# Kernel tuning notes

Measured on AMD Instinct MI355X. Metric: run time of the kernel, lower is better.

## Reference

```python
import jax, jax.numpy as jnp
import numpy as np

H = 16  # n_heads

def setup_inputs() -> dict:
    key = jax.random.key(0)
    ks = jax.random.split(key, 11)
    B, L, D = 2, 2048, 1024
    w = 1.0 / np.sqrt(D).astype(np.float32)
    return {
        "query": jax.random.normal(ks[0], (B, L, D), jnp.float32),
        "key":   jax.random.normal(ks[1], (B, L, D), jnp.float32),
        "value": jax.random.normal(ks[2], (B, L, D), jnp.float32),
        "Wq": jax.random.normal(ks[3], (D, D), jnp.float32) * w,
        "bq": jax.random.normal(ks[4], (D,), jnp.float32) * 0.01,
        "Wk": jax.random.normal(ks[5], (D, D), jnp.float32) * w,
        "bk": jax.random.normal(ks[6], (D,), jnp.float32) * 0.01,
        "Wv": jax.random.normal(ks[7], (D, D), jnp.float32) * w,
        "bv": jax.random.normal(ks[8], (D,), jnp.float32) * 0.01,
        "Wo": jax.random.normal(ks[9], (D, D), jnp.float32) * w,
        "bo": jax.random.normal(ks[10], (D,), jnp.float32) * 0.01,
        "masksize": 256,
    }

def reference(query, key, value, Wq, bq, Wk, bk, Wv, bv, Wo, bo, masksize):
    B, L, D = query.shape
    d_k = D // H
    scale = 1.0 / np.sqrt(d_k).astype(np.float32)

    def proj(x, W, b):
        # nn.Linear: x @ W.T + b, then [B,L,H,d_k] -> [B,H,L,d_k]
        return (x @ W.T + b).reshape(B, L, H, d_k).transpose(0, 2, 1, 3)

    q = proj(query, Wq, bq)
    k = proj(key, Wk, bk)
    v = proj(value, Wv, bv)

    # Sliding-window float mask (faithful to original: a 0/1 FLOAT tensor is
    # passed as attn_mask to SDPA, so it is ADDED to scores, not -inf-masked).
    half = masksize // 2
    i = jnp.arange(L)[:, None]
    j = jnp.arange(L)[None, :]
    band = (jnp.abs(i - j) <= half).astype(q.dtype)  # [L, L]

    scores = jnp.einsum('bhqd,bhkd->bhqk', q, k) * scale + band  # [B,H,L,L]
    attn = jax.nn.softmax(scores, axis=-1)
    out = jnp.einsum('bhqk,bhkd->bhqd', attn, v)  # [B,H,L,d_k]
    out = out.transpose(0, 2, 1, 3).reshape(B, L, D)
    return out @ Wo.T + bo
```

## Files before the change

kernel.cpp:

```cpp
#include <hip/hip_runtime.h>
#include <hip/hip_bf16.h>

#define Hh 16
#define Ll 2048
#define Dd 1024
#define DK 64
#define Mm 4096
#define Kk 1024
#define Nn 1024

typedef short bf16x8 __attribute__((ext_vector_type(8)));
typedef float f32x4 __attribute__((ext_vector_type(4)));

static __device__ __forceinline__ unsigned short f2bf(float f) {
    union { __hip_bfloat16 b; unsigned short u; } cv;
    cv.b = __float2bfloat16(f);
    return cv.u;
}

static __device__ __forceinline__ unsigned packtr(float a, float b) {
    return __builtin_amdgcn_perm(__builtin_bit_cast(unsigned, b),
                                 __builtin_bit_cast(unsigned, a), 0x07060302u);
}

static __device__ __forceinline__ float fexp2(float x) {
    return __builtin_amdgcn_exp2f(x);
}

static __device__ __forceinline__ void glds16(const ushort* g, ushort* l) {
    __builtin_amdgcn_global_load_lds((const __attribute__((address_space(1))) unsigned int*)g,
                                     (__attribute__((address_space(3))) unsigned int*)l,
                                     16, 0, 0);
}

__global__ __launch_bounds__(256) void cast_all(
    const float* __restrict__ q, const float* __restrict__ k, const float* __restrict__ v,
    const float* __restrict__ wq, const float* __restrict__ wk, const float* __restrict__ wv,
    const float* __restrict__ wo,
    ushort* __restrict__ qb, ushort* __restrict__ kb, ushort* __restrict__ vb,
    ushort* __restrict__ wqb, ushort* __restrict__ wkb, ushort* __restrict__ wvb,
    ushort* __restrict__ wob) {
    const int bx = blockIdx.x;
    const float4* s; ushort4* d; int base;
    if      (bx <  4096) { s = (const float4*)q;  d = (ushort4*)qb;  base = 0; }
    else if (bx <  8192) { s = (const float4*)k;  d = (ushort4*)kb;  base = 4096; }
    else if (bx < 12288) { s = (const float4*)v;  d = (ushort4*)vb;  base = 8192; }
    else if (bx < 13312) { s = (const float4*)wq; d = (ushort4*)wqb; base = 12288; }
    else if (bx < 14336) { s = (const float4*)wk; d = (ushort4*)wkb; base = 13312; }
    else if (bx < 15360) { s = (const float4*)wv; d = (ushort4*)wvb; base = 14336; }
    else                 { s = (const float4*)wo; d = (ushort4*)wob; base = 15360; }
    const int i = (bx - base) * 256 + threadIdx.x;
    float4 vv = s[i];
    ushort4 o;
    o.x = f2bf(vv.x); o.y = f2bf(vv.y); o.z = f2bf(vv.z); o.w = f2bf(vv.w);
    d[i] = o;
}

__global__ __launch_bounds__(256) void gemm_qkv(
    const ushort* __restrict__ A0, const ushort* __restrict__ A1, const ushort* __restrict__ A2,
    const ushort* __restrict__ W0, const ushort* __restrict__ W1, const ushort* __restrict__ W2,
    const float* __restrict__ b0, const float* __restrict__ b1, const float* __restrict__ b2,
    ushort* __restrict__ O0, ushort* __restrict__ O1, ushort* __restrict__ OVt) {
    __shared__ __align__(16) ushort SM[2 * 128 * 32];
    ushort* As = SM;
    ushort* Bs = SM + 4096;

    const int fl = blockIdx.x;
    const int xcd = fl & 7, bcoli = (fl >> 3) & 7, slot = fl >> 6;
    const int g = slot * 8 + xcd;
    const int z = g >> 5;
    const int browi = g & 31;

    const ushort* A = (z == 0) ? A0 : (z == 1) ? A1 : A2;
    const ushort* W = (z == 0) ? W0 : (z == 1) ? W1 : W2;
    const float* bias = (z == 0) ? b0 : (z == 1) ? b1 : b2;

    const int t = threadIdx.x;
    const int wave = t >> 6, lane = t & 63;
    const int quad = lane >> 4, l15 = lane & 15;
    const int brow = browi * 128, bcol = bcoli * 128;
    const int wr = (wave >> 1) * 64, wc = (wave & 1) * 64;
    const int gr = wave * 16 + (lane >> 2);
    const int gc = (lane & 3) * 8;

    f32x4 acc[4][4] = {};

    for (int k0 = 0; k0 < Kk; k0 += 32) {
        __syncthreads();
        glds16(A + (size_t)(brow + gr) * Kk + k0 + gc,      As + wave * 512);
        glds16(A + (size_t)(brow + 64 + gr) * Kk + k0 + gc, As + 2048 + wave * 512);
        glds16(W + (size_t)(bcol + gr) * Kk + k0 + gc,      Bs + wave * 512);
        glds16(W + (size_t)(bcol + 64 + gr) * Kk + k0 + gc, Bs + 2048 + wave * 512);
        __syncthreads();

        bf16x8 af[4], bfr[4];
#pragma unroll
        for (int i = 0; i < 4; i++)
            af[i] = *(const bf16x8*)(As + (wr + i * 16 + l15) * 32 + quad * 8);
#pragma unroll
        for (int j = 0; j < 4; j++)
            bfr[j] = *(const bf16x8*)(Bs + (wc + j * 16 + l15) * 32 + quad * 8);
#pragma unroll
        for (int i = 0; i < 4; i++)
#pragma unroll
            for (int j = 0; j < 4; j++)
                acc[i][j] = __builtin_amdgcn_mfma_f32_16x16x32_bf16(af[i], bfr[j], acc[i][j], 0, 0, 0);
    }

    if (z < 2) {
        ushort* Out = (z == 0) ? O0 : O1;
        const float oscl = (z == 0) ? 0.18033688f : 1.0f;
        const int b = brow >> 11;
        const int lbase = (brow & 2047) + wr;
        const int h = (bcol + wc) >> 6;
        ushort* T = SM + wave * 1280;
        __syncthreads();
#pragma unroll
        for (int i = 0; i < 4; i++) {
#pragma unroll
            for (int j = 0; j < 4; j++) {
                const float bv = bias[bcol + wc + j * 16 + l15];
#pragma unroll
                for (int r = 0; r < 4; r++)
                    T[(quad * 4 + r) * 80 + j * 16 + l15] = f2bf((acc[i][j][r] + bv) * oscl);
            }
            const int r8 = lane >> 3, c8 = lane & 7;
#pragma unroll
            for (int pass = 0; pass < 2; pass++) {
                const uint4 val = *(const uint4*)(T + (pass * 8 + r8) * 80 + c8 * 8);
                const int l = lbase + i * 16 + pass * 8 + r8;
                *(uint4*)(Out + ((size_t)(b * Hh + h) * Ll + l) * DK + c8 * 8) = val;
            }
        }
    } else {
        ushort* T = SM;
        const int b = brow >> 11;
        const int lbase = brow & 2047;
        const int npr = (wave & 1) * 16 + l15;
#pragma unroll
        for (int j = 0; j < 4; j++) {
            __syncthreads();
            const float bv = bias[bcol + wc + j * 16 + l15];
#pragma unroll
            for (int i = 0; i < 4; i++)
#pragma unroll
                for (int r = 0; r < 4; r++) {
                    const int m = wr + i * 16 + quad * 4 + r;
                    T[npr * 136 + m] = f2bf(acc[i][j][r] + bv);
                }
            __syncthreads();
#pragma unroll
            for (int cc = 0; cc < 2; cc++) {
                const int idx = t + cc * 256;
                const int ni = idx >> 4;
                const int ms = idx & 15;
                const int n = bcol + (ni >> 4) * 64 + j * 16 + (ni & 15);
                const int hh = n >> 6, dk = n & 63;
                uint4 val = *(const uint4*)(T + ni * 136 + ms * 8);
                *(uint4*)(OVt + ((size_t)(b * Hh + hh) * DK + dk) * Ll + lbase + ms * 8) = val;
            }
        }
    }
}

__global__ __launch_bounds__(256) void attn_kernel(const ushort* __restrict__ Q,
                                                   const ushort* __restrict__ Kp,
                                                   const ushort* __restrict__ Vt,
                                                   ushort* __restrict__ Oout,
                                                   const int* __restrict__ masksize) {
    __shared__ __align__(16) ushort Ks[2 * 128 * 32];
    __shared__ __align__(16) ushort Vs[64 * 128];
    const int t = threadIdx.x;
    const int wave = t >> 6, lane = t & 63;
    const int quad = lane >> 4, l15 = lane & 15;
    const int bx = blockIdx.x;
    const int bh = bx & 31, qc = bx >> 5;
    const int q0w = qc * 128 + wave * 32;
    const int half = masksize[0] >> 1;
    const unsigned wid = (unsigned)(2 * half);

    const ushort* Qb = Q + (size_t)bh * (Ll * DK);
    const ushort* Kb = Kp + (size_t)bh * (Ll * DK);
    const ushort* Vb = Vt + (size_t)bh * (DK * Ll);

    const bf16x8 qA0 = *(const bf16x8*)(Qb + (size_t)(q0w + l15) * DK + quad * 8);
    const bf16x8 qA1 = *(const bf16x8*)(Qb + (size_t)(q0w + l15) * DK + 32 + quad * 8);
    const bf16x8 qB0 = *(const bf16x8*)(Qb + (size_t)(q0w + 16 + l15) * DK + quad * 8);
    const bf16x8 qB1 = *(const bf16x8*)(Qb + (size_t)(q0w + 16 + l15) * DK + 32 + quad * 8);

    const float C2IN  = (1.0f - 24.0f) * 1.44269504088896f;
    const float C2OUT = -24.0f * 1.44269504088896f;
    const float E1 = 2.718281828f;

    bf16x8 onesf;
#pragma unroll
    for (int j = 0; j < 8; j++) onesf[j] = (short)0x3F80;

    f32x4 OA[4] = {}, OB[4] = {};
    f32x4 SA = {}, SB = {};

    const int krow = lane >> 2;
    const int kcol8 = (lane & 3) * 8;
    const int vdl = lane >> 4;
    const int vg0 = 2 * (lane & 15);

    for (int kt = 0; kt < Ll; kt += 128) {
        __syncthreads();
        if (wave < 2) {
            const int cbase = wave * 4;
#pragma unroll
            for (int c = 0; c < 4; c++)
#pragma unroll
                for (int pan = 0; pan < 2; pan++)
                    glds16(Kb + (size_t)(kt + (cbase + c) * 16 + krow) * DK + pan * 32 + kcol8,
                           Ks + (pan * 128 + (cbase + c) * 16) * 32);
        } else {
            const int sb = (wave - 2) * 8;
#pragma unroll
            for (int i = 0; i < 8; i++) {
                const int sidx = sb + i;
                const int d = sidx * 4 + vdl;
                const int g0 = vg0 ^ (d & 30);
                glds16(Vb + (size_t)d * Ll + kt + g0 * 4, Vs + sidx * 512);
            }
        }
        __syncthreads();

        const int qlo = q0w, qhi = q0w + 31;
        const bool allout = (kt + 127 < qlo - half) || (kt > qhi + half);
        const bool allin  = (kt >= qhi - half) && (kt + 127 <= qlo + half);
        const bool uniform = allin || allout;
        const float cinit = allin ? C2IN : C2OUT;
        f32x4 cvec = {cinit, cinit, cinit, cinit};

#pragma unroll
        for (int s = 0; s < 4; s++) {
            const bf16x8 kf00 = *(const bf16x8*)(Ks + ((2 * s) * 16 + l15) * 32 + quad * 8);
            const bf16x8 kf01 = *(const bf16x8*)(Ks + 4096 + ((2 * s) * 16 + l15) * 32 + quad * 8);
            const bf16x8 kf10 = *(const bf16x8*)(Ks + ((2 * s + 1) * 16 + l15) * 32 + quad * 8);
            const bf16x8 kf11 = *(const bf16x8*)(Ks + 4096 + ((2 * s + 1) * 16 + l15) * 32 + quad * 8);
            f32x4 zA0 = __builtin_amdgcn_mfma_f32_16x16x32_bf16(kf00, qA0, cvec, 0, 0, 0);
            zA0 = __builtin_amdgcn_mfma_f32_16x16x32_bf16(kf01, qA1, zA0, 0, 0, 0);
            f32x4 zA1 = __builtin_amdgcn_mfma_f32_16x16x32_bf16(kf10, qA0, cvec, 0, 0, 0);
            zA1 = __builtin_amdgcn_mfma_f32_16x16x32_bf16(kf11, qA1, zA1, 0, 0, 0);
            f32x4 zB0 = __builtin_amdgcn_mfma_f32_16x16x32_bf16(kf00, qB0, cvec, 0, 0, 0);
            zB0 = __builtin_amdgcn_mfma_f32_16x16x32_bf16(kf01, qB1, zB0, 0, 0, 0);
            f32x4 zB1 = __builtin_amdgcn_mfma_f32_16x16x32_bf16(kf10, qB0, cvec, 0, 0, 0);
            zB1 = __builtin_amdgcn_mfma_f32_16x16x32_bf16(kf11, qB1, zB1, 0, 0, 0);

            float pA[8], pB[8];
            if (uniform) {
#pragma unroll
                for (int g = 0; g < 2; g++)
#pragma unroll
                    for (int r = 0; r < 4; r++) {
                        pA[g * 4 + r] = fexp2(g ? zA1[r] : zA0[r]);
                        pB[g * 4 + r] = fexp2(g ? zB1[r] : zB0[r]);
                    }
            } else {
                const int kb = kt + s * 32 + quad * 4 + half;
#pragma unroll
                for (int g = 0; g < 2; g++)
#pragma unroll
                    for (int r = 0; r < 4; r++) {
                        const unsigned ttA = (unsigned)(kb + g * 16 + r - (q0w + l15));
                        const unsigned ttB = (unsigned)(kb + g * 16 + r - (q0w + 16 + l15));
                        pA[g * 4 + r] = fexp2(g ? zA1[r] : zA0[r]) * (ttA <= wid ? E1 : 1.0f);
                        pB[g * 4 + r] = fexp2(g ? zB1[r] : zB0[r]) * (ttB <= wid ? E1 : 1.0f);
                    }
            }

            bf16x8 pfA, pfB;
            ((unsigned*)&pfA)[0] = packtr(pA[0], pA[1]);
            ((unsigned*)&pfA)[1] = packtr(pA[2], pA[3]);
            ((unsigned*)&pfA)[2] = packtr(pA[4], pA[5]);
            ((unsigned*)&pfA)[3] = packtr(pA[6], pA[7]);
            ((unsigned*)&pfB)[0] = packtr(pB[0], pB[1]);
            ((unsigned*)&pfB)[1] = packtr(pB[2], pB[3]);
            ((unsigned*)&pfB)[2] = packtr(pB[4], pB[5]);
            ((unsigned*)&pfB)[3] = packtr(pB[6], pB[7]);

            SA = __builtin_amdgcn_mfma_f32_16x16x32_bf16(pfA, onesf, SA, 0, 0, 0);
            SB = __builtin_amdgcn_mfma_f32_16x16x32_bf16(pfB, onesf, SB, 0, 0, 0);

#pragma unroll
            for (int i = 0; i < 4; i++) {
                const int d = i * 16 + l15;
                const int x4 = (d & 30) * 4;
                const int bi = d * 128;
                const ushort4 v1 = *(const ushort4*)(Vs + bi + (((s * 8 + quad) * 4) ^ x4));
                const ushort4 v2 = *(const ushort4*)(Vs + bi + (((s * 8 + 4 + quad) * 4) ^ x4));
                bf16x8 vc;
                *(ushort4*)&vc = v1;
                *((ushort4*)&vc + 1) = v2;
                OA[i] = __builtin_amdgcn_mfma_f32_16x16x32_bf16(pfA, vc, OA[i], 0, 0, 0);
                OB[i] = __builtin_amdgcn_mfma_f32_16x16x32_bf16(pfB, vc, OB[i], 0, 0, 0);
            }
        }
    }

    float liA[4], liB[4];
#pragma unroll
    for (int r = 0; r < 4; r++) {
        liA[r] = 1.0f / SA[r];
        liB[r] = 1.0f / SB[r];
    }

    const int b = bh >> 4, h = bh & 15;
#pragma unroll
    for (int i = 0; i < 4; i++)
#pragma unroll
        for (int r = 0; r < 4; r++) {
            const int qa = q0w + quad * 4 + r;
            Oout[((size_t)b * Ll + qa) * Dd + h * DK + i * 16 + l15] = f2bf(OA[i][r] * liA[r]);
            Oout[((size_t)b * Ll + qa + 16) * Dd + h * DK + i * 16 + l15] = f2bf(OB[i][r] * liB[r]);
        }
}

__global__ __launch_bounds__(256) void gemm_o(const ushort* __restrict__ A,
                                              const ushort* __restrict__ W,
                                              const float* __restrict__ bias,
                                              float* __restrict__ Out) {
    __shared__ __align__(16) ushort As[64 * 32];
    __shared__ __align__(16) ushort Bs[128 * 32];
    const int fl = blockIdx.x;
    const int xcd = fl & 7, bcoli = (fl >> 3) & 7, slot = fl >> 6;
    const int g = slot * 8 + xcd;
    const int t = threadIdx.x;
    const int wave = t >> 6, lane = t & 63;
    const int quad = lane >> 4, l15 = lane & 15;
    const int brow = g * 64, bcol = bcoli * 128;
    const int wr = (wave >> 1) * 32, wc = (wave & 1) * 64;
    const int gr = wave * 16 + (lane >> 2);
    const int gc = (lane & 3) * 8;

    f32x4 acc[2][4] = {};

    for (int k0 = 0; k0 < Kk; k0 += 32) {
        __syncthreads();
        glds16(A + (size_t)(brow + gr) * Kk + k0 + gc,      As + wave * 512);
        glds16(W + (size_t)(bcol + gr) * Kk + k0 + gc,      Bs + wave * 512);
        glds16(W + (size_t)(bcol + 64 + gr) * Kk + k0 + gc, Bs + 2048 + wave * 512);
        __syncthreads();

        bf16x8 af[2], bfr[4];
#pragma unroll
        for (int i = 0; i < 2; i++)
            af[i] = *(const bf16x8*)(As + (wr + i * 16 + l15) * 32 + quad * 8);
#pragma unroll
        for (int j = 0; j < 4; j++)
            bfr[j] = *(const bf16x8*)(Bs + (wc + j * 16 + l15) * 32 + quad * 8);
#pragma unroll
        for (int i = 0; i < 2; i++)
#pragma unroll
            for (int j = 0; j < 4; j++)
                acc[i][j] = __builtin_amdgcn_mfma_f32_16x16x32_bf16(af[i], bfr[j], acc[i][j], 0, 0, 0);
    }

#pragma unroll
    for (int i = 0; i < 2; i++)
#pragma unroll
        for (int j = 0; j < 4; j++) {
            const int n = bcol + wc + j * 16 + l15;
            const float bv = bias[n];
#pragma unroll
            for (int r = 0; r < 4; r++) {
                const int m = brow + wr + i * 16 + quad * 4 + r;
                Out[(size_t)m * Nn + n] = acc[i][j][r] + bv;
            }
        }
}

extern "C" void kernel_launch(void* const* d_in, const int* in_sizes, int n_in,
                              void* d_out, int out_size, void* d_ws, size_t ws_size,
                              hipStream_t stream) {
    const float* query = (const float*)d_in[0];
    const float* key   = (const float*)d_in[1];
    const float* value = (const float*)d_in[2];
    const float* Wq = (const float*)d_in[3];
    const float* bq = (const float*)d_in[4];
    const float* Wk = (const float*)d_in[5];
    const float* bk = (const float*)d_in[6];
    const float* Wv = (const float*)d_in[7];
    const float* bv = (const float*)d_in[8];
    const float* Wo = (const float*)d_in[9];
    const float* bo = (const float*)d_in[10];
    const int* masksize = (const int*)d_in[11];

    char* ws = (char*)d_ws;
    const size_t MB = 1024 * 1024;
    ushort* qb  = (ushort*)(ws + 0 * MB);
    ushort* kbf = (ushort*)(ws + 8 * MB);
    ushort* vbf = (ushort*)(ws + 16 * MB);
    ushort* wqb = (ushort*)(ws + 24 * MB);
    ushort* wkb = (ushort*)(ws + 26 * MB);
    ushort* wvb = (ushort*)(ws + 28 * MB);
    ushort* wob = (ushort*)(ws + 30 * MB);
    ushort* Qp  = (ushort*)(ws + 32 * MB);
    ushort* Kp  = (ushort*)(ws + 40 * MB);
    ushort* Vt  = (ushort*)(ws + 48 * MB);
    ushort* AO  = (ushort*)(ws + 56 * MB);

    cast_all<<<16384, 256, 0, stream>>>(query, key, value, Wq, Wk, Wv, Wo,
                                        qb, kbf, vbf, wqb, wkb, wvb, wob);

    gemm_qkv<<<768, 256, 0, stream>>>(qb, kbf, vbf,
                                      wqb, wkb, wvb,
                                      bq, bk, bv,
                                      Qp, Kp, Vt);

    attn_kernel<<<512, 256, 0, stream>>>(Qp, Kp, Vt, AO, masksize);

    gemm_o<<<512, 256, 0, stream>>>(AO, wob, bo, (float*)d_out);
}
```

Before: 219.5 us.

## Double-buffer LDS tiles in attention and output-projection kernels

Splits the K/V shared-memory tiles in the attention kernel and the A/W tiles in the output GEMM into two buffers. The next tile's async global-to-LDS loads are issued before computing on the current tile, so each iteration needs one barrier instead of two and load latency can overlap with MFMA work. This doubles LDS use per block, which may lower occupancy. Correctness depends on the single trailing barrier also covering completion of the async loads.

```diff
diff --git a/kernel.cpp b/kernel.cpp
--- a/kernel.cpp
+++ b/kernel.cpp
@@ -168,8 +168,8 @@
                                                    const ushort* __restrict__ Vt,
                                                    ushort* __restrict__ Oout,
                                                    const int* __restrict__ masksize) {
-    __shared__ __align__(16) ushort Ks[2 * 128 * 32];
-    __shared__ __align__(16) ushort Vs[64 * 128];
+    __shared__ __align__(16) ushort Ks[2][2 * 128 * 32];
+    __shared__ __align__(16) ushort Vs[2][64 * 128];
     const int t = threadIdx.x;
     const int wave = t >> 6, lane = t & 63;
     const int quad = lane >> 4, l15 = lane & 15;
@@ -204,27 +204,35 @@
     const int vdl = lane >> 4;
     const int vg0 = 2 * (lane & 15);
 
+#define STAGE(buf, kt0) do {                                                           \
+    if (wave < 2) {                                                                    \
+        const int cbase = wave * 4;                                                    \
+        _Pragma("unroll")                                                              \
+        for (int c = 0; c < 4; c++)                                                    \
+            _Pragma("unroll")                                                          \
+            for (int pan = 0; pan < 2; pan++)                                          \
+                glds16(Kb + (size_t)((kt0) + (cbase + c) * 16 + krow) * DK + pan * 32 + kcol8, \
+                       Ks[buf] + (pan * 128 + (cbase + c) * 16) * 32);                 \
+    } else {                                                                           \
+        const int sb = (wave - 2) * 8;                                                 \
+        _Pragma("unroll")                                                              \
+        for (int i = 0; i < 8; i++) {                                                  \
+            const int sidx = sb + i;                                                   \
+            const int d = sidx * 4 + vdl;                                              \
+            const int g0 = vg0 ^ (d & 30);                                             \
+            glds16(Vb + (size_t)d * Ll + (kt0) + g0 * 4, Vs[buf] + sidx * 512);        \
+        }                                                                              \
+    }                                                                                  \
+} while (0)
+
+    STAGE(0, 0);
+    __syncthreads();
+    int cur = 0;
+
     for (int kt = 0; kt < Ll; kt += 128) {
-        __syncthreads();
-        if (wave < 2) {
-            const int cbase = wave * 4;
-#pragma unroll
-            for (int c = 0; c < 4; c++)
-#pragma unroll
-                for (int pan = 0; pan < 2; pan++)
-                    glds16(Kb + (size_t)(kt + (cbase + c) * 16 + krow) * DK + pan * 32 + kcol8,
-                           Ks + (pan * 128 + (cbase + c) * 16) * 32);
-        } else {
-            const int sb = (wave - 2) * 8;
-#pragma unroll
-            for (int i = 0; i < 8; i++) {
-                const int sidx = sb + i;
-                const int d = sidx * 4 + vdl;
-                const int g0 = vg0 ^ (d & 30);
-                glds16(Vb + (size_t)d * Ll + kt + g0 * 4, Vs + sidx * 512);
-            }
-        }
-        __syncthreads();
+        if (kt + 128 < Ll) STAGE(cur ^ 1, kt + 128);
+        const ushort* Kc = Ks[cur];
+        const ushort* Vc = Vs[cur];
 
         const int qlo = q0w, qhi = q0w + 31;
         const bool allout = (kt + 127 < qlo - half) || (kt > qhi + half);
@@ -235,10 +243,10 @@
 
 #pragma unroll
         for (int s = 0; s < 4; s++) {
-            const bf16x8 kf00 = *(const bf16x8*)(Ks + ((2 * s) * 16 + l15) * 32 + quad * 8);
-            const bf16x8 kf01 = *(const bf16x8*)(Ks + 4096 + ((2 * s) * 16 + l15) * 32 + quad * 8);
-            const bf16x8 kf10 = *(const bf16x8*)(Ks + ((2 * s + 1) * 16 + l15) * 32 + quad * 8);
-            const bf16x8 kf11 = *(const bf16x8*)(Ks + 4096 + ((2 * s + 1) * 16 + l15) * 32 + quad * 8);
+            const bf16x8 kf00 = *(const bf16x8*)(Kc + ((2 * s) * 16 + l15) * 32 + quad * 8);
+            const bf16x8 kf01 = *(const bf16x8*)(Kc + 4096 + ((2 * s) * 16 + l15) * 32 + quad * 8);
+            const bf16x8 kf10 = *(const bf16x8*)(Kc + ((2 * s + 1) * 16 + l15) * 32 + quad * 8);
+            const bf16x8 kf11 = *(const bf16x8*)(Kc + 4096 + ((2 * s + 1) * 16 + l15) * 32 + quad * 8);
             f32x4 zA0 = __builtin_amdgcn_mfma_f32_16x16x32_bf16(kf00, qA0, cvec, 0, 0, 0);
             zA0 = __builtin_amdgcn_mfma_f32_16x16x32_bf16(kf01, qA1, zA0, 0, 0, 0);
             f32x4 zA1 = __builtin_amdgcn_mfma_f32_16x16x32_bf16(kf10, qA0, cvec, 0, 0, 0);
@@ -288,8 +296,8 @@
                 const int d = i * 16 + l15;
                 const int x4 = (d & 30) * 4;
                 const int bi = d * 128;
-                const ushort4 v1 = *(const ushort4*)(Vs + bi + (((s * 8 + quad) * 4) ^ x4));
-                const ushort4 v2 = *(const ushort4*)(Vs + bi + (((s * 8 + 4 + quad) * 4) ^ x4));
+                const ushort4 v1 = *(const ushort4*)(Vc + bi + (((s * 8 + quad) * 4) ^ x4));
+                const ushort4 v2 = *(const ushort4*)(Vc + bi + (((s * 8 + 4 + quad) * 4) ^ x4));
                 bf16x8 vc;
                 *(ushort4*)&vc = v1;
                 *((ushort4*)&vc + 1) = v2;
@@ -297,7 +305,10 @@
                 OB[i] = __builtin_amdgcn_mfma_f32_16x16x32_bf16(pfB, vc, OB[i], 0, 0, 0);
             }
         }
+        __syncthreads();
+        cur ^= 1;
     }
+#undef STAGE
 
     float liA[4], liB[4];
 #pragma unroll
@@ -321,8 +332,8 @@
                                               const ushort* __restrict__ W,
                                               const float* __restrict__ bias,
                                               float* __restrict__ Out) {
-    __shared__ __align__(16) ushort As[64 * 32];
-    __shared__ __align__(16) ushort Bs[128 * 32];
+    __shared__ __align__(16) ushort As[2][64 * 32];
+    __shared__ __align__(16) ushort Bs[2][128 * 32];
     const int fl = blockIdx.x;
     const int xcd = fl & 7, bcoli = (fl >> 3) & 7, slot = fl >> 6;
     const int g = slot * 8 + xcd;
@@ -336,26 +347,34 @@
 
     f32x4 acc[2][4] = {};
 
+#define OSTAGE(buf, k0) do {                                                         \
+    glds16(A + (size_t)(brow + gr) * Kk + (k0) + gc,      As[buf] + wave * 512);     \
+    glds16(W + (size_t)(bcol + gr) * Kk + (k0) + gc,      Bs[buf] + wave * 512);     \
+    glds16(W + (size_t)(bcol + 64 + gr) * Kk + (k0) + gc, Bs[buf] + 2048 + wave * 512); \
+} while (0)
+
+    OSTAGE(0, 0);
+    __syncthreads();
+    int cur = 0;
+
     for (int k0 = 0; k0 < Kk; k0 += 32) {
-        __syncthreads();
-        glds16(A + (size_t)(brow + gr) * Kk + k0 + gc,      As + wave * 512);
-        glds16(W + (size_t)(bcol + gr) * Kk + k0 + gc,      Bs + wave * 512);
-        glds16(W + (size_t)(bcol + 64 + gr) * Kk + k0 + gc, Bs + 2048 + wave * 512);
-        __syncthreads();
-
+        if (k0 + 32 < Kk) OSTAGE(cur ^ 1, k0 + 32);
         bf16x8 af[2], bfr[4];
 #pragma unroll
         for (int i = 0; i < 2; i++)
-            af[i] = *(const bf16x8*)(As + (wr + i * 16 + l15) * 32 + quad * 8);
+            af[i] = *(const bf16x8*)(As[cur] + (wr + i * 16 + l15) * 32 + quad * 8);
 #pragma unroll
         for (int j = 0; j < 4; j++)
-            bfr[j] = *(const bf16x8*)(Bs + (wc + j * 16 + l15) * 32 + quad * 8);
+            bfr[j] = *(const bf16x8*)(Bs[cur] + (wc + j * 16 + l15) * 32 + quad * 8);
 #pragma unroll
         for (int i = 0; i < 2; i++)
 #pragma unroll
             for (int j = 0; j < 4; j++)
                 acc[i][j] = __builtin_amdgcn_mfma_f32_16x16x32_bf16(af[i], bfr[j], acc[i][j], 0, 0, 0);
+        __syncthreads();
+        cur ^= 1;
     }
+#undef OSTAGE
 
 #pragma unroll
     for (int i = 0; i < 2; i++)
```

New measurement: 218.5 us. Within noise of the previous version (-0.5%).
